# Optimization experiments

Measured on AMD Instinct MI355X. Metric: run time of the kernel, lower is better.

Reference implementation:

```python
import jax, jax.numpy as jnp
import numpy as np

TEMPERATURE = 0.5

def setup_inputs() -> dict:
    key = jax.random.key(0)
    k1, k2 = jax.random.split(key)
    emb_i = jax.random.normal(k1, (4096, 128), dtype=jnp.float32)
    emb_j = jax.random.normal(k2, (4096, 128), dtype=jnp.float32)
    return {"emb_i": emb_i, "emb_j": emb_j}

def reference(emb_i, emb_j):
    B = emb_i.shape[0]
    eps = 1e-12
    z_i = emb_i / jnp.maximum(jnp.linalg.norm(emb_i, axis=1, keepdims=True), eps)
    z_j = emb_j / jnp.maximum(jnp.linalg.norm(emb_j, axis=1, keepdims=True), eps)
    z = jnp.concatenate([z_i, z_j], axis=0)  # [2B, D]
    # cosine similarity of normalized vectors == dot product (GEMM instead of O(N^2 D) broadcast)
    sim = z @ z.T  # [2B, 2B]
    sim_ij = jnp.einsum('bd,bd->b', z_i, z_j)  # diag(sim, +B)
    positives = jnp.concatenate([sim_ij, sim_ij], axis=0)  # diag(sim,-B) == diag(sim,+B)
    neg_mask = 1.0 - jnp.eye(2 * B, dtype=sim.dtype)
    denom = jnp.sum(neg_mask * jnp.exp(sim / TEMPERATURE), axis=1)  # [2B]
    loss_partial = -(positives / TEMPERATURE - jnp.log(denom))
    return jnp.sum(loss_partial) / (2 * B)
```

## Files before the change

### kernel.cpp

```cpp
#include <hip/hip_runtime.h>
#include <hip/hip_bf16.h>
#include <math.h>

#define BB       4096
#define N2       8192
#define DIMS     128
#define WAVES    4
#define ROWTILES 4
#define ROWS_PER_WAVE   64
#define ROWS_PER_BLOCK  256
#define COL_SPLIT       16
#define COLS_PER_BLOCK  (N2 / COL_SPLIT)
#define CHUNK    64
#define LDS_PAD  8
#define LDS_ROWW (DIMS + LDS_PAD)

#define ZSCALE   1.6986436f
#define DIAG_E2  7.38905609893065f

typedef __attribute__((ext_vector_type(8))) short short8;
typedef __attribute__((ext_vector_type(4))) float float4v;

__global__ __launch_bounds__(256) void norm_kernel(
    const float* __restrict__ emb_i, const float* __restrict__ emb_j,
    __hip_bfloat16* __restrict__ z, float* __restrict__ pos,
    float* __restrict__ denom) {
  if (blockIdx.x < N2 / 256) denom[blockIdx.x * 256 + threadIdx.x] = 0.0f;

  int gw   = (blockIdx.x * blockDim.x + threadIdx.x) >> 6;
  int lane = threadIdx.x & 63;
  if (gw >= BB) return;

  const float2* ei = (const float2*)(emb_i + (size_t)gw * DIMS);
  const float2* ej = (const float2*)(emb_j + (size_t)gw * DIMS);
  float2 a = ei[lane];
  float2 b = ej[lane];

  float sa = a.x * a.x + a.y * a.y;
  float sb = b.x * b.x + b.y * b.y;
  #pragma unroll
  for (int m = 32; m; m >>= 1) {
    sa += __shfl_xor(sa, m, 64);
    sb += __shfl_xor(sb, m, 64);
  }
  float inva = 1.0f / fmaxf(sqrtf(sa), 1e-12f);
  float invb = 1.0f / fmaxf(sqrtf(sb), 1e-12f);

  float zi0 = a.x * inva, zi1 = a.y * inva;
  float zj0 = b.x * invb, zj1 = b.y * invb;

  float p = zi0 * zj0 + zi1 * zj1;
  #pragma unroll
  for (int m = 32; m; m >>= 1) p += __shfl_xor(p, m, 64);
  if (lane == 0) pos[gw] = p;

  __hip_bfloat162* zr_i = (__hip_bfloat162*)(z + (size_t)gw * DIMS);
  __hip_bfloat162* zr_j = (__hip_bfloat162*)(z + (size_t)(gw + BB) * DIMS);
  __hip_bfloat162 vi, vj;
  vi.x = __float2bfloat16(zi0 * ZSCALE); vi.y = __float2bfloat16(zi1 * ZSCALE);
  vj.x = __float2bfloat16(zj0 * ZSCALE); vj.y = __float2bfloat16(zj1 * ZSCALE);
  zr_i[lane] = vi;
  zr_j[lane] = vj;
}

__global__ __launch_bounds__(256, 2) void simloss_main(
    const __hip_bfloat16* __restrict__ z, float* __restrict__ denom) {
  const int blk      = blockIdx.x;
  const int rowBlk   = blk >> 4;
  const int colBlk   = blk & 15;
  const int rowBase  = rowBlk * ROWS_PER_BLOCK;
  const int colBase0 = colBlk * COLS_PER_BLOCK;
  const int tid  = threadIdx.x;
  const int wave = tid >> 6;
  const int lane = tid & 63;
  const int lr   = lane & 15;
  const int quad = lane >> 4;

  __shared__ short lds[CHUNK * LDS_ROWW];

  const ushort* zp = (const ushort*)z;

  short8 afrag[ROWTILES][4];
  #pragma unroll
  for (int rt = 0; rt < ROWTILES; rt++) {
    const int arow = rowBase + wave * ROWS_PER_WAVE + rt * 16 + lr;
    const short8* ap = (const short8*)(zp + (size_t)arow * DIMS + quad * 8);
    afrag[rt][0] = ap[0];
    afrag[rt][1] = ap[4];
    afrag[rt][2] = ap[8];
    afrag[rt][3] = ap[12];
  }

  float rowsum[ROWTILES][4];
  #pragma unroll
  for (int rt = 0; rt < ROWTILES; rt++)
    #pragma unroll
    for (int r = 0; r < 4; r++) rowsum[rt][r] = 0.0f;

  for (int cc = 0; cc < COLS_PER_BLOCK; cc += CHUNK) {
    const int colBase = colBase0 + cc;

    __syncthreads();
    {
      const short8* src = (const short8*)(zp + (size_t)colBase * DIMS);
      #pragma unroll
      for (int i = 0; i < 4; i++) {
        int idx  = tid + 256 * i;
        int row  = idx >> 4;
        int col8 = idx & 15;
        *(short8*)&lds[row * LDS_ROWW + col8 * 8] = src[idx];
      }
    }
    __syncthreads();

    #pragma unroll
    for (int t = 0; t < 4; t++) {
      const short8* bp = (const short8*)&lds[(t * 16 + lr) * LDS_ROWW + quad * 8];
      short8 b0 = bp[0];
      short8 b1 = bp[4];
      short8 b2 = bp[8];
      short8 b3 = bp[12];
      #pragma unroll
      for (int rt = 0; rt < ROWTILES; rt++) {
        float4v acc = {0.0f, 0.0f, 0.0f, 0.0f};
        acc = __builtin_amdgcn_mfma_f32_16x16x32_bf16(afrag[rt][0], b0, acc, 0, 0, 0);
        acc = __builtin_amdgcn_mfma_f32_16x16x32_bf16(afrag[rt][1], b1, acc, 0, 0, 0);
        acc = __builtin_amdgcn_mfma_f32_16x16x32_bf16(afrag[rt][2], b2, acc, 0, 0, 0);
        acc = __builtin_amdgcn_mfma_f32_16x16x32_bf16(afrag[rt][3], b3, acc, 0, 0, 0);
        #pragma unroll
        for (int r = 0; r < 4; r++)
          rowsum[rt][r] += __builtin_amdgcn_exp2f(acc[r]);
      }
    }
  }

  #pragma unroll
  for (int m = 1; m < 16; m <<= 1) {
    #pragma unroll
    for (int rt = 0; rt < ROWTILES; rt++)
      #pragma unroll
      for (int r = 0; r < 4; r++)
        rowsum[rt][r] += __shfl_xor(rowsum[rt][r], m, 64);
  }
  if (lr == 0) {
    #pragma unroll
    for (int rt = 0; rt < ROWTILES; rt++)
      #pragma unroll
      for (int r = 0; r < 4; r++)
        atomicAdd(&denom[rowBase + wave * ROWS_PER_WAVE + rt * 16 + quad * 4 + r],
                  rowsum[rt][r]);
  }
}

__global__ __launch_bounds__(256) void finalize(
    const float* __restrict__ denom, const float* __restrict__ pos,
    float* __restrict__ out) {
  __shared__ double sred[256];
  int tid = threadIdx.x;
  double acc = 0.0;
  for (int r = tid; r < N2; r += 256) {
    acc += (double)(logf(denom[r] - DIAG_E2) - 2.0f * pos[r & (BB - 1)]);
  }
  sred[tid] = acc;
  __syncthreads();
  for (int s = 128; s; s >>= 1) {
    if (tid < s) sred[tid] += sred[tid + s];
    __syncthreads();
  }
  if (tid == 0) out[0] = (float)(sred[0] / (double)N2);
}

extern "C" void kernel_launch(void* const* d_in, const int* in_sizes, int n_in,
                              void* d_out, int out_size, void* d_ws, size_t ws_size,
                              hipStream_t stream) {
  const float* emb_i = (const float*)d_in[0];
  const float* emb_j = (const float*)d_in[1];

  __hip_bfloat16* z = (__hip_bfloat16*)d_ws;
  float* pos   = (float*)((char*)d_ws + (size_t)N2 * DIMS * 2);
  float* denom = (float*)((char*)pos + BB * sizeof(float));

  norm_kernel<<<BB / 4, 256, 0, stream>>>(emb_i, emb_j, z, pos, denom);
  simloss_main<<<(N2 / ROWS_PER_BLOCK) * COL_SPLIT, 256, 0, stream>>>(z, denom);
  finalize<<<1, 256, 0, stream>>>(denom, pos, (float*)d_out);
}
```

Baseline: 92.01 us.

## Enlarge row tiles, stage full column slab in swizzled LDS, fuse finalize via counter

Each block now covers 512 rows × 256 columns and loads its whole 64KB column slab into LDS once, using an XOR swizzle in place of padding. Each wave holds 8 A row-tiles in registers, which doubles reuse of every B fragment read from LDS and removes the per-chunk barriers. The separate finalize kernel is folded into the main kernel: the last block to finish, detected with an atomic counter and a threadfence, does the log-sum reduction, saving a launch. The trade-offs are higher register use (8×4 short8 A fragments), which may cut occupancy below the 2 blocks per CU requested by the launch bounds, and a final reduction that runs serially in a single block.

```diff
diff --git a/kernel.cpp b/kernel.cpp
--- a/kernel.cpp
+++ b/kernel.cpp
@@ -6,14 +6,12 @@
 #define N2       8192
 #define DIMS     128
 #define WAVES    4
-#define ROWTILES 4
-#define ROWS_PER_WAVE   64
-#define ROWS_PER_BLOCK  256
-#define COL_SPLIT       16
-#define COLS_PER_BLOCK  (N2 / COL_SPLIT)
-#define CHUNK    64
-#define LDS_PAD  8
-#define LDS_ROWW (DIMS + LDS_PAD)
+#define ROWTILES 8
+#define ROWS_PER_WAVE   128
+#define ROWS_PER_BLOCK  512
+#define COL_SPLIT       32
+#define COLS_PER_BLOCK  256
+#define GRID            512
 
 #define ZSCALE   1.6986436f
 #define DIAG_E2  7.38905609893065f
@@ -24,8 +22,9 @@
 __global__ __launch_bounds__(256) void norm_kernel(
     const float* __restrict__ emb_i, const float* __restrict__ emb_j,
     __hip_bfloat16* __restrict__ z, float* __restrict__ pos,
-    float* __restrict__ denom) {
+    float* __restrict__ denom, unsigned int* __restrict__ counter) {
   if (blockIdx.x < N2 / 256) denom[blockIdx.x * 256 + threadIdx.x] = 0.0f;
+  if (blockIdx.x == 32 && threadIdx.x == 0) *counter = 0u;
 
   int gw   = (blockIdx.x * blockDim.x + threadIdx.x) >> 6;
   int lane = threadIdx.x & 63;
@@ -64,21 +63,34 @@
 }
 
 __global__ __launch_bounds__(256, 2) void simloss_main(
-    const __hip_bfloat16* __restrict__ z, float* __restrict__ denom) {
-  const int blk      = blockIdx.x;
-  const int rowBlk   = blk >> 4;
-  const int colBlk   = blk & 15;
-  const int rowBase  = rowBlk * ROWS_PER_BLOCK;
-  const int colBase0 = colBlk * COLS_PER_BLOCK;
+    const __hip_bfloat16* __restrict__ z, float* __restrict__ denom,
+    const float* __restrict__ pos, float* __restrict__ out,
+    unsigned int* __restrict__ counter) {
+  const int blk     = blockIdx.x;
+  const int rowBase = (blk >> 5) * ROWS_PER_BLOCK;
+  const int colBase = (blk & 31) * COLS_PER_BLOCK;
   const int tid  = threadIdx.x;
   const int wave = tid >> 6;
   const int lane = tid & 63;
   const int lr   = lane & 15;
   const int quad = lane >> 4;
 
-  __shared__ short lds[CHUNK * LDS_ROWW];
+  __shared__ short lds[COLS_PER_BLOCK * DIMS];
 
   const ushort* zp = (const ushort*)z;
+
+  {
+    const short8* src = (const short8*)(zp + (size_t)colBase * DIMS);
+    #pragma unroll 4
+    for (int i = 0; i < 16; i++) {
+      int idx  = tid + 256 * i;
+      int row  = idx >> 4;
+      int col8 = idx & 15;
+      int sw   = col8 ^ (row & 15);
+      *(short8*)&lds[row * DIMS + sw * 8] = src[idx];
+    }
+  }
+  __syncthreads();
 
   short8 afrag[ROWTILES][4];
   #pragma unroll
@@ -97,40 +109,24 @@
     #pragma unroll
     for (int r = 0; r < 4; r++) rowsum[rt][r] = 0.0f;
 
-  for (int cc = 0; cc < COLS_PER_BLOCK; cc += CHUNK) {
-    const int colBase = colBase0 + cc;
-
-    __syncthreads();
-    {
-      const short8* src = (const short8*)(zp + (size_t)colBase * DIMS);
+  for (int t = 0; t < 16; t++) {
+    const int row = t * 16 + lr;
+    short8 bkk[4];
+    #pragma unroll
+    for (int kk = 0; kk < 4; kk++) {
+      int col8 = (kk * 4 + quad) ^ lr;
+      bkk[kk] = *(const short8*)&lds[row * DIMS + col8 * 8];
+    }
+    #pragma unroll
+    for (int rt = 0; rt < ROWTILES; rt++) {
+      float4v acc = {0.0f, 0.0f, 0.0f, 0.0f};
+      acc = __builtin_amdgcn_mfma_f32_16x16x32_bf16(afrag[rt][0], bkk[0], acc, 0, 0, 0);
+      acc = __builtin_amdgcn_mfma_f32_16x16x32_bf16(afrag[rt][1], bkk[1], acc, 0, 0, 0);
+      acc = __builtin_amdgcn_mfma_f32_16x16x32_bf16(afrag[rt][2], bkk[2], acc, 0, 0, 0);
+      acc = __builtin_amdgcn_mfma_f32_16x16x32_bf16(afrag[rt][3], bkk[3], acc, 0, 0, 0);
       #pragma unroll
-      for (int i = 0; i < 4; i++) {
-        int idx  = tid + 256 * i;
-        int row  = idx >> 4;
-        int col8 = idx & 15;
-        *(short8*)&lds[row * LDS_ROWW + col8 * 8] = src[idx];
-      }
-    }
-    __syncthreads();
-
-    #pragma unroll
-    for (int t = 0; t < 4; t++) {
-      const short8* bp = (const short8*)&lds[(t * 16 + lr) * LDS_ROWW + quad * 8];
-      short8 b0 = bp[0];
-      short8 b1 = bp[4];
-      short8 b2 = bp[8];
-      short8 b3 = bp[12];
-      #pragma unroll
-      for (int rt = 0; rt < ROWTILES; rt++) {
-        float4v acc = {0.0f, 0.0f, 0.0f, 0.0f};
-        acc = __builtin_amdgcn_mfma_f32_16x16x32_bf16(afrag[rt][0], b0, acc, 0, 0, 0);
-        acc = __builtin_amdgcn_mfma_f32_16x16x32_bf16(afrag[rt][1], b1, acc, 0, 0, 0);
-        acc = __builtin_amdgcn_mfma_f32_16x16x32_bf16(afrag[rt][2], b2, acc, 0, 0, 0);
-        acc = __builtin_amdgcn_mfma_f32_16x16x32_bf16(afrag[rt][3], b3, acc, 0, 0, 0);
-        #pragma unroll
-        for (int r = 0; r < 4; r++)
-          rowsum[rt][r] += __builtin_amdgcn_exp2f(acc[r]);
-      }
+      for (int r = 0; r < 4; r++)
+        rowsum[rt][r] += __builtin_amdgcn_exp2f(acc[r]);
     }
   }
 
@@ -150,24 +146,31 @@
         atomicAdd(&denom[rowBase + wave * ROWS_PER_WAVE + rt * 16 + quad * 4 + r],
                   rowsum[rt][r]);
   }
-}
 
-__global__ __launch_bounds__(256) void finalize(
-    const float* __restrict__ denom, const float* __restrict__ pos,
-    float* __restrict__ out) {
-  __shared__ double sred[256];
-  int tid = threadIdx.x;
-  double acc = 0.0;
-  for (int r = tid; r < N2; r += 256) {
-    acc += (double)(logf(denom[r] - DIAG_E2) - 2.0f * pos[r & (BB - 1)]);
+  __threadfence();
+  __syncthreads();
+  if (tid == 0) {
+    unsigned int old = atomicAdd(counter, 1u);
+    *(int*)&lds[0] = (old == GRID - 1) ? 1 : 0;
   }
-  sred[tid] = acc;
   __syncthreads();
-  for (int s = 128; s; s >>= 1) {
-    if (tid < s) sred[tid] += sred[tid + s];
+  if (*(int*)&lds[0]) {
+    __threadfence();
+    double acc = 0.0;
+    for (int r = tid; r < N2; r += 256) {
+      float d = __hip_atomic_load(&denom[r], __ATOMIC_RELAXED,
+                                  __HIP_MEMORY_SCOPE_AGENT);
+      acc += (double)(logf(d - DIAG_E2) - 2.0f * pos[r & (BB - 1)]);
+    }
+    double* sred = (double*)lds;
+    sred[tid] = acc;
     __syncthreads();
+    for (int s = 128; s; s >>= 1) {
+      if (tid < s) sred[tid] += sred[tid + s];
+      __syncthreads();
+    }
+    if (tid == 0) out[0] = (float)(sred[0] / (double)N2);
   }
-  if (tid == 0) out[0] = (float)(sred[0] / (double)N2);
 }
 
 extern "C" void kernel_launch(void* const* d_in, const int* in_sizes, int n_in,
@@ -179,8 +182,8 @@
   __hip_bfloat16* z = (__hip_bfloat16*)d_ws;
   float* pos   = (float*)((char*)d_ws + (size_t)N2 * DIMS * 2);
   float* denom = (float*)((char*)pos + BB * sizeof(float));
+  unsigned int* counter = (unsigned int*)((char*)denom + N2 * sizeof(float));
 
-  norm_kernel<<<BB / 4, 256, 0, stream>>>(emb_i, emb_j, z, pos, denom);
-  simloss_main<<<(N2 / ROWS_PER_BLOCK) * COL_SPLIT, 256, 0, stream>>>(z, denom);
-  finalize<<<1, 256, 0, stream>>>(denom, pos, (float*)d_out);
+  norm_kernel<<<BB / 4, 256, 0, stream>>>(emb_i, emb_j, z, pos, denom, counter);
+  simloss_main<<<GRID, 256, 0, stream>>>(z, denom, pos, (float*)d_out, counter);
 }
```

Result: slower. 115.6 us (+25.6%).

## Load whole 128-column B tile once with XOR-swizzled LDS, raise occupancy

Applied to the files above, without the earlier changes.

Each block now covers a single 128-column tile instead of looping over 512 columns in 64-column chunks, so the grid grows from 512 to 2048 blocks. The full B tile is loaded into LDS once and only one barrier is needed. Padding is replaced by an XOR swizzle to avoid bank conflicts, and launch bounds request 4 blocks per CU. The trade-off is that A fragments are reloaded four times as often and there are four times as many atomic adds into denom.

```diff
diff --git a/kernel.cpp b/kernel.cpp
--- a/kernel.cpp
+++ b/kernel.cpp
@@ -9,11 +9,9 @@
 #define ROWTILES 4
 #define ROWS_PER_WAVE   64
 #define ROWS_PER_BLOCK  256
-#define COL_SPLIT       16
-#define COLS_PER_BLOCK  (N2 / COL_SPLIT)
-#define CHUNK    64
-#define LDS_PAD  8
-#define LDS_ROWW (DIMS + LDS_PAD)
+#define COLS_PER_BLOCK  128
+#define COL_SPLIT       (N2 / COLS_PER_BLOCK)
+#define GRID            ((N2 / ROWS_PER_BLOCK) * COL_SPLIT)
 
 #define ZSCALE   1.6986436f
 #define DIAG_E2  7.38905609893065f
@@ -63,20 +61,18 @@
   zr_j[lane] = vj;
 }
 
-__global__ __launch_bounds__(256, 2) void simloss_main(
+__global__ __launch_bounds__(256, 4) void simloss_main(
     const __hip_bfloat16* __restrict__ z, float* __restrict__ denom) {
-  const int blk      = blockIdx.x;
-  const int rowBlk   = blk >> 4;
-  const int colBlk   = blk & 15;
-  const int rowBase  = rowBlk * ROWS_PER_BLOCK;
-  const int colBase0 = colBlk * COLS_PER_BLOCK;
+  const int blk     = blockIdx.x;
+  const int rowBase = (blk >> 6) * ROWS_PER_BLOCK;
+  const int colBase = (blk & 63) * COLS_PER_BLOCK;
   const int tid  = threadIdx.x;
   const int wave = tid >> 6;
   const int lane = tid & 63;
   const int lr   = lane & 15;
   const int quad = lane >> 4;
 
-  __shared__ short lds[CHUNK * LDS_ROWW];
+  __shared__ short lds[COLS_PER_BLOCK * DIMS];
 
   const ushort* zp = (const ushort*)z;
 
@@ -91,46 +87,44 @@
     afrag[rt][3] = ap[12];
   }
 
+  {
+    const short8* src = (const short8*)(zp + (size_t)colBase * DIMS);
+    #pragma unroll
+    for (int i = 0; i < 8; i++) {
+      int idx  = tid + 256 * i;
+      int row  = idx >> 4;
+      int col8 = idx & 15;
+      int sw   = col8 ^ (row & 15);
+      *(short8*)&lds[row * DIMS + sw * 8] = src[idx];
+    }
+  }
+  __syncthreads();
+
   float rowsum[ROWTILES][4];
   #pragma unroll
   for (int rt = 0; rt < ROWTILES; rt++)
     #pragma unroll
     for (int r = 0; r < 4; r++) rowsum[rt][r] = 0.0f;
 
-  for (int cc = 0; cc < COLS_PER_BLOCK; cc += CHUNK) {
-    const int colBase = colBase0 + cc;
-
-    __syncthreads();
-    {
-      const short8* src = (const short8*)(zp + (size_t)colBase * DIMS);
+  #pragma unroll
+  for (int t = 0; t < 8; t++) {
+    const int row = t * 16 + lr;
+    short8 bkk[4];
+    #pragma unroll
+    for (int kk = 0; kk < 4; kk++) {
+      int col8 = (kk * 4 + quad) ^ lr;
+      bkk[kk] = *(const short8*)&lds[row * DIMS + col8 * 8];
+    }
+    #pragma unroll
+    for (int rt = 0; rt < ROWTILES; rt++) {
+      float4v acc = {0.0f, 0.0f, 0.0f, 0.0f};
+      acc = __builtin_amdgcn_mfma_f32_16x16x32_bf16(afrag[rt][0], bkk[0], acc, 0, 0, 0);
+      acc = __builtin_amdgcn_mfma_f32_16x16x32_bf16(afrag[rt][1], bkk[1], acc, 0, 0, 0);
+      acc = __builtin_amdgcn_mfma_f32_16x16x32_bf16(afrag[rt][2], bkk[2], acc, 0, 0, 0);
+      acc = __builtin_amdgcn_mfma_f32_16x16x32_bf16(afrag[rt][3], bkk[3], acc, 0, 0, 0);
       #pragma unroll
-      for (int i = 0; i < 4; i++) {
-        int idx  = tid + 256 * i;
-        int row  = idx >> 4;
-        int col8 = idx & 15;
-        *(short8*)&lds[row * LDS_ROWW + col8 * 8] = src[idx];
-      }
-    }
-    __syncthreads();
-
-    #pragma unroll
-    for (int t = 0; t < 4; t++) {
-      const short8* bp = (const short8*)&lds[(t * 16 + lr) * LDS_ROWW + quad * 8];
-      short8 b0 = bp[0];
-      short8 b1 = bp[4];
-      short8 b2 = bp[8];
-      short8 b3 = bp[12];
-      #pragma unroll
-      for (int rt = 0; rt < ROWTILES; rt++) {
-        float4v acc = {0.0f, 0.0f, 0.0f, 0.0f};
-        acc = __builtin_amdgcn_mfma_f32_16x16x32_bf16(afrag[rt][0], b0, acc, 0, 0, 0);
-        acc = __builtin_amdgcn_mfma_f32_16x16x32_bf16(afrag[rt][1], b1, acc, 0, 0, 0);
-        acc = __builtin_amdgcn_mfma_f32_16x16x32_bf16(afrag[rt][2], b2, acc, 0, 0, 0);
-        acc = __builtin_amdgcn_mfma_f32_16x16x32_bf16(afrag[rt][3], b3, acc, 0, 0, 0);
-        #pragma unroll
-        for (int r = 0; r < 4; r++)
-          rowsum[rt][r] += __builtin_amdgcn_exp2f(acc[r]);
-      }
+      for (int r = 0; r < 4; r++)
+        rowsum[rt][r] += __builtin_amdgcn_exp2f(acc[r]);
     }
   }
 
@@ -181,6 +175,6 @@
   float* denom = (float*)((char*)pos + BB * sizeof(float));
 
   norm_kernel<<<BB / 4, 256, 0, stream>>>(emb_i, emb_j, z, pos, denom);
-  simloss_main<<<(N2 / ROWS_PER_BLOCK) * COL_SPLIT, 256, 0, stream>>>(z, denom);
+  simloss_main<<<GRID, 256, 0, stream>>>(z, denom);
   finalize<<<1, 256, 0, stream>>>(denom, pos, (float*)d_out);
 }
```

New measurement: 109.3 us. 1.19x slower.
